# Kernel optimization log

Measured on AMD Instinct MI355X. Metric: run time of the kernel, lower is better.

Reference implementation:

```python
import jax, jax.numpy as jnp
import numpy as np

ALPHA = 0.15  # top-k fraction (forward default)


def setup_inputs() -> dict:
    key = jax.random.key(0)
    k1, k2, k3 = jax.random.split(key, 3)
    B, N, D = 8, 1024, 256
    x = jax.random.normal(k1, (B, N, D), dtype=jnp.float32)
    # torch nn.Linear(dim, H*head_dim, bias=False); stored here as [D, H*head_dim]
    W_src = jax.random.normal(k2, (D, D), dtype=jnp.float32) * (1.0 / np.sqrt(D))
    W_tgt = jax.random.normal(k3, (D, D), dtype=jnp.float32) * (1.0 / np.sqrt(D))
    return {"x": x, "W_src": W_src, "W_tgt": W_tgt}


def _topk_mask(adj, k):
    # adj: [B,H,N,N]; exact scatter of 1.0 at top-k indices along last axis
    B, H, N, _ = adj.shape
    _, idx = jax.lax.top_k(adj, k)              # [B,H,N,k]
    bi = jnp.arange(B)[:, None, None, None]
    hi = jnp.arange(H)[None, :, None, None]
    ni = jnp.arange(N)[None, None, :, None]
    mask = jnp.zeros_like(adj).at[bi, hi, ni, idx].set(1.0)
    return mask


def reference(x, W_src, W_tgt):
    # directed=True path of DirectedGraphLearner.forward
    B, N, D = x.shape
    H, head_dim = 4, D // 4
    k = max(1, int(ALPHA * N))
    src = (x @ W_src).reshape(B, N, H, head_dim)
    tgt = (x @ W_tgt).reshape(B, N, H, head_dim)
    adj = jnp.einsum('bihd,bjhd->bhij', src, tgt)
    adj = jax.nn.gelu(adj, approximate=False)    # torch F.gelu default = exact erf
    mask = _topk_mask(adj, k)
    return adj * mask
```

## Files before the change

kernel.cpp:

```cpp
#include <hip/hip_runtime.h>
#include <math.h>


#define KSEL 153u
#define EPSK 61000u

typedef __attribute__((ext_vector_type(8))) short short8v;
typedef __attribute__((ext_vector_type(4))) float float4v;

__device__ __forceinline__ float gelu_f32(float x) {
    return 0.5f * x * (1.0f + erff(x * 0.70710678118654752f));
}

__device__ __forceinline__ unsigned long long d2key(double v) {
    unsigned long long u = (unsigned long long)__double_as_longlong(v);
    return (u >> 63) ? ~u : (u | 0x8000000000000000ull);
}

__device__ __forceinline__ unsigned lkeyf(float v) {
    float q = fmaf(v, 33554432.0f, 2147483648.0f);
    q = fminf(fmaxf(q, 0.0f), 4294967040.0f);
    return (unsigned)q;
}

__device__ __forceinline__ unsigned short b16(float x) {
    unsigned u = __float_as_uint(x);
    u += 0x7FFFu + ((u >> 16) & 1u);
    return (unsigned short)(u >> 16);
}
__device__ __forceinline__ float bf2f(unsigned short h) {
    return __uint_as_float(((unsigned)h) << 16);
}
__device__ __forceinline__ unsigned pk2(float a, float b) {
    return (unsigned)b16(a) | ((unsigned)b16(b) << 16);
}

#define LGKM0()                                             \
    do {                                                    \
        asm volatile("s_waitcnt lgkmcnt(0)" ::: "memory");  \
        __builtin_amdgcn_sched_barrier(0);                  \
    } while (0)

template <bool W32>
__global__ __launch_bounds__(256) void k1_proj(const float* __restrict__ x,
                                               const float* __restrict__ Wsrc,
                                               const float* __restrict__ Wtgt,
                                               double* __restrict__ ws,
                                               unsigned short* __restrict__ th,
                                               unsigned short* __restrict__ tl) {
    __shared__ float xs[32 * 68];
    __shared__ float wsh[32 * 68];
    const int t = threadIdx.x;
    const int bx = blockIdx.x;
    const int by = blockIdx.y;
    const int col0 = (by & 3) * 64;
    const float* __restrict__ W = (by < 4) ? Wsrc : Wtgt;
    double* __restrict__ outp = ws + ((by < 4) ? 0 : 2097152);

    double acc[4][4];
#pragma unroll
    for (int i = 0; i < 4; ++i)
#pragma unroll
        for (int j = 0; j < 4; ++j) acc[i][j] = 0.0;

    const int m_loc = (t & 15) * 4;
    const int c_loc = (t >> 4) * 4;

    for (int kt = 0; kt < 8; ++kt) {
        __syncthreads();
#pragma unroll
        for (int it = 0; it < 2; ++it) {
            int f4 = t + 256 * it;
            int m = f4 >> 3, k4 = f4 & 7;
            float4 v = *reinterpret_cast<const float4*>(&x[(bx * 64 + m) * 256 + kt * 32 + 4 * k4]);
            xs[(4 * k4 + 0) * 68 + m] = v.x;
            xs[(4 * k4 + 1) * 68 + m] = v.y;
            xs[(4 * k4 + 2) * 68 + m] = v.z;
            xs[(4 * k4 + 3) * 68 + m] = v.w;
        }
#pragma unroll
        for (int it = 0; it < 2; ++it) {
            int f4 = t + 256 * it;
            int k = f4 >> 4, c4 = f4 & 15;
            *reinterpret_cast<float4*>(&wsh[k * 68 + 4 * c4]) =
                *reinterpret_cast<const float4*>(&W[(kt * 32 + k) * 256 + col0 + 4 * c4]);
        }
        __syncthreads();
#pragma unroll
        for (int kk = 0; kk < 32; ++kk) {
            float4 a = *reinterpret_cast<const float4*>(&xs[kk * 68 + m_loc]);
            float4 b = *reinterpret_cast<const float4*>(&wsh[kk * 68 + c_loc]);
            double ad[4] = {a.x, a.y, a.z, a.w};
            double bd[4] = {b.x, b.y, b.z, b.w};
#pragma unroll
            for (int i = 0; i < 4; ++i)
#pragma unroll
                for (int j = 0; j < 4; ++j) acc[i][j] += ad[i] * bd[j];
        }
    }
    const int hd = by & 3;
#pragma unroll
    for (int i = 0; i < 4; ++i) {
        int m = bx * 64 + m_loc + i;
        int b = m >> 10, n = m & 1023;
        int bhd = b * 4 + hd;
        size_t base = ((size_t)(bhd * 1024 + n)) * 64 + c_loc;
        double2 v01, v23;
        v01.x = acc[i][0]; v01.y = acc[i][1];
        v23.x = acc[i][2]; v23.y = acc[i][3];
        *reinterpret_cast<double2*>(&outp[base]) = v01;
        *reinterpret_cast<double2*>(&outp[base + 2]) = v23;
        if (W32 && by >= 4) {
            float f0 = (float)acc[i][0], f1 = (float)acc[i][1];
            float f2 = (float)acc[i][2], f3 = (float)acc[i][3];
            unsigned short h0 = b16(f0), h1 = b16(f1), h2 = b16(f2), h3 = b16(f3);
            uint2 H, L;
            H.x = (unsigned)h0 | ((unsigned)h1 << 16);
            H.y = (unsigned)h2 | ((unsigned)h3 << 16);
            L.x = pk2(f0 - bf2f(h0), f1 - bf2f(h1));
            L.y = pk2(f2 - bf2f(h2), f3 - bf2f(h3));
            int T = n >> 4, colLow = n & 15;
            int ks = c_loc >> 5, kg = (c_loc >> 3) & 3, elem = c_loc & 7;
            size_t fidx = ((size_t)bhd * 65536) +
                          (size_t)(((T * 2 + ks) * 64 + kg * 16 + colLow) * 8 + elem);
            *reinterpret_cast<uint2*>(&th[fidx]) = H;
            *reinterpret_cast<uint2*>(&tl[fidx]) = L;
        }
    }
}

template <bool FAST>
__global__ __launch_bounds__(256, 4) void k2a_gemm(const double* __restrict__ srcT,
                                                   const double* __restrict__ tgtT,
                                                   const unsigned short* __restrict__ th,
                                                   const unsigned short* __restrict__ tlo,
                                                   float* __restrict__ out) {
    __shared__ __align__(16) float tr[16 * 512];

    unsigned short* sHI = reinterpret_cast<unsigned short*>(tr);
    unsigned short* sLO = sHI + 1024;

    const int t = threadIdx.x;
    const int lane = t & 63;
    const int wv = t >> 6;
    const int bid = (blockIdx.x & 7) * 256 + (blockIdx.x >> 3);
    const int bh = bid >> 6;
    const int itile = bid & 63;
    const int row0 = itile * 16;
    const int r0 = 4 * wv;
    const size_t tgtBase = (size_t)bh * 65536;
    const unsigned short* __restrict__ thb = th + tgtBase;
    const unsigned short* __restrict__ tlb = tlo + tgtBase;

    {
        int r = t >> 4, dq = (t & 15) * 4;
        const double* sp = &srcT[((size_t)bh * 1024 + row0 + r) * 64 + dq];
        double2 a = *reinterpret_cast<const double2*>(sp);
        double2 b = *reinterpret_cast<const double2*>(sp + 2);
        float f0 = (float)a.x, f1 = (float)a.y, f2 = (float)b.x, f3 = (float)b.y;
        unsigned short h0 = b16(f0), h1 = b16(f1), h2 = b16(f2), h3 = b16(f3);
        int s = dq >> 3;
        int idx = r * 64 + ((s ^ (r & 7)) << 3) + (dq & 7);
        uint2 H, L;
        H.x = (unsigned)h0 | ((unsigned)h1 << 16);
        H.y = (unsigned)h2 | ((unsigned)h3 << 16);
        L.x = pk2(f0 - bf2f(h0), f1 - bf2f(h1));
        L.y = pk2(f2 - bf2f(h2), f3 - bf2f(h3));
        *reinterpret_cast<uint2*>(&sHI[idx]) = H;
        *reinterpret_cast<uint2*>(&sLO[idx]) = L;
    }
    __syncthreads();

    short8v Ah[2], Al[2];
#pragma unroll
    for (int ks = 0; ks < 2; ++ks) {
        int idxA = (lane & 15) * 64 + (((4 * ks + (lane >> 4)) ^ (lane & 7)) << 3);
        Ah[ks] = *reinterpret_cast<const short8v*>(&sHI[idxA]);
        Al[ks] = *reinterpret_cast<const short8v*>(&sLO[idxA]);
    }

    const int colA = lane & 15;
    const int kgrp = lane >> 4;
    const size_t outBase = ((size_t)bh * 1024 + row0 + r0) * 1024;

#pragma unroll
    for (int h = 0; h < 2; ++h) {
        float4v acc[8];
#pragma unroll
        for (int a = 0; a < 8; ++a) acc[a] = (float4v){0.f, 0.f, 0.f, 0.f};

#pragma unroll
        for (int u = 0; u < 8; ++u) {
            const int T = 32 * h + 4 * u + wv;
#pragma unroll
            for (int ks = 0; ks < 2; ++ks) {
                short8v Bh, Bl;
                if (FAST) {
                    const size_t fbase = (size_t)(((T * 2 + ks) * 64 + lane) * 8);
                    Bh = *reinterpret_cast<const short8v*>(&thb[fbase]);
                    Bl = *reinterpret_cast<const short8v*>(&tlb[fbase]);
                } else {
                    const size_t cbase = (size_t)(16 * T + colA) * 64 + kgrp * 8;
                    const double* gp = &tgtT[tgtBase + cbase + 32 * ks];
                    double2 d0 = *reinterpret_cast<const double2*>(gp);
                    double2 d1 = *reinterpret_cast<const double2*>(gp + 2);
                    double2 d2 = *reinterpret_cast<const double2*>(gp + 4);
                    double2 d3 = *reinterpret_cast<const double2*>(gp + 6);
                    float f[8] = {(float)d0.x, (float)d0.y, (float)d1.x, (float)d1.y,
                                  (float)d2.x, (float)d2.y, (float)d3.x, (float)d3.y};
                    unsigned short hh[8];
#pragma unroll
                    for (int e = 0; e < 8; ++e) hh[e] = b16(f[e]);
                    unsigned Hw[4], Lw[4];
#pragma unroll
                    for (int e = 0; e < 4; ++e) {
                        Hw[e] = (unsigned)hh[2 * e] | ((unsigned)hh[2 * e + 1] << 16);
                        Lw[e] = pk2(f[2 * e] - bf2f(hh[2 * e]), f[2 * e + 1] - bf2f(hh[2 * e + 1]));
                    }
                    Bh = *reinterpret_cast<const short8v*>(Hw);
                    Bl = *reinterpret_cast<const short8v*>(Lw);
                }
                acc[u] = __builtin_amdgcn_mfma_f32_16x16x32_bf16(Ah[ks], Bh, acc[u], 0, 0, 0);
                acc[u] = __builtin_amdgcn_mfma_f32_16x16x32_bf16(Al[ks], Bh, acc[u], 0, 0, 0);
                acc[u] = __builtin_amdgcn_mfma_f32_16x16x32_bf16(Ah[ks], Bl, acc[u], 0, 0, 0);
            }
        }

        __syncthreads();
#pragma unroll
        for (int u = 0; u < 8; ++u) {
            int colh = 16 * (4 * u + wv) + colA;
#pragma unroll
            for (int reg = 0; reg < 4; ++reg) {
                int row = 4 * kgrp + reg;
                tr[row * 512 + (colh ^ ((kgrp & 1) << 4))] = acc[u][reg];
            }
        }
        __syncthreads();
        const int rsw = (wv & 1) << 4;
#pragma unroll
        for (int ri = 0; ri < 4; ++ri) {
            int row = r0 + ri;
#pragma unroll
            for (int mm = 0; mm < 8; ++mm) {
                int colh = lane + 64 * mm;
                out[outBase + (size_t)ri * 1024 + 512 * h + colh] =
                    tr[row * 512 + (colh ^ rsw)];
            }
        }
    }
}

__global__ __launch_bounds__(256, 4) void k2b_select(const double* __restrict__ srcT,
                                                     const double* __restrict__ tgtT,
                                                     float* __restrict__ out) {
    __shared__ __align__(16) unsigned hist[4][256];

    const int t = threadIdx.x;
    const int lane = t & 63;
    const int wv = t >> 6;
    const int R = blockIdx.x * 4 + wv;
    const int bh = R >> 10;
    const size_t tgtBase = (size_t)bh * 65536;
    const size_t base = (size_t)R * 1024;

    float vals[16];
#pragma unroll
    for (int m = 0; m < 16; ++m) vals[m] = out[base + lane + 64 * m];

    unsigned* histw = hist[wv];
    unsigned* cjp = histw + 128;
    unsigned long long* ckp = reinterpret_cast<unsigned long long*>(histw);
    unsigned* ccp = histw + 192;

    unsigned ul[16];
#pragma unroll
    for (int m = 0; m < 16; ++m) ul[m] = lkeyf(vals[m]);

    unsigned prefA = 0u, maskA = 0u, rk = KSEL;
#pragma unroll 1
    for (int p = 1; p >= 0; --p) {
        const int sh = 16 + 8 * p;
        *reinterpret_cast<uint4*>(&histw[4 * lane]) = make_uint4(0u, 0u, 0u, 0u);
        LGKM0();
#pragma unroll
        for (int m = 0; m < 16; ++m) {
            if ((ul[m] & maskA) == prefA)
                atomicAdd(&histw[(ul[m] >> sh) & 255u], 1u);
        }
        LGKM0();
        unsigned h0 = histw[4 * lane + 0], h1 = histw[4 * lane + 1];
        unsigned h2 = histw[4 * lane + 2], h3 = histw[4 * lane + 3];
        unsigned S = h0 + h1 + h2 + h3;
        unsigned inc = S;
#pragma unroll
        for (int off = 1; off < 64; off <<= 1) {
            unsigned o = __shfl_down(inc, off, 64);
            inc = (lane + off < 64) ? (inc + o) : inc;
        }
        unsigned above = inc - S;
        bool found = (above < rk) && (rk <= inc);
        unsigned long long bal = __ballot(found);
        int L = __ffsll(bal) - 1;
        unsigned hh[4];
        hh[0] = __shfl(h0, L, 64);
        hh[1] = __shfl(h1, L, 64);
        hh[2] = __shfl(h2, L, 64);
        hh[3] = __shfl(h3, L, 64);
        unsigned cum = __shfl(above, L, 64);
        int bsel = -1;
#pragma unroll
        for (int q = 3; q >= 0; --q) {
            if (bsel < 0) {
                if (rk <= cum + hh[q]) {
                    bsel = q;
                    rk = rk - cum;
                } else {
                    cum += hh[q];
                }
            }
        }
        prefA |= (unsigned)(4 * L + bsel) << sh;
        maskA |= 0xFFu << sh;
    }

    const unsigned klo = prefA - EPSK;
    const unsigned khi = prefA + 65535u + EPSK;

    int ch = 0, cb = 0;
#pragma unroll
    for (int m = 0; m < 16; ++m) {
        ch += (ul[m] > khi) ? 1 : 0;
        cb += (ul[m] >= klo && ul[m] <= khi) ? 1 : 0;
    }
#pragma unroll
    for (int off = 32; off; off >>= 1) {
        ch += __shfl_xor(ch, off, 64);
        cb += __shfl_xor(cb, off, 64);
    }
    const unsigned need = KSEL - (unsigned)ch;
    const bool fastp = ((unsigned)cb == need);

    unsigned long long selMask = 0ull;
    unsigned cidx[16];
    if (!fastp) {
        if (lane == 0) *ccp = 0u;
        LGKM0();
#pragma unroll
        for (int m = 0; m < 16; ++m) {
            cidx[m] = 0xFFFFFFFFu;
            if (ul[m] >= klo && ul[m] <= khi) {
                unsigned idx = atomicAdd(ccp, 1u);
                cidx[m] = idx;
                if (idx < 64u) cjp[idx] = (unsigned)(lane + 64 * m);
            }
        }
        LGKM0();
        unsigned g = *ccp;
        if (g > 64u) g = 64u;
        unsigned rnk = need;
        if (lane < (int)g) {
            unsigned j = cjp[lane];
            const double2* sp = reinterpret_cast<const double2*>(&srcT[(size_t)R * 64]);
            const double2* tp = reinterpret_cast<const double2*>(&tgtT[tgtBase + (size_t)j * 64]);
            double a2 = 0.0;
#pragma unroll 8
            for (int d2 = 0; d2 < 32; ++d2) {
                double2 aa = sp[d2], bb = tp[d2];
                a2 = fma(aa.x, bb.x, fma(aa.y, bb.y, a2));
            }
            ckp[lane] = d2key(a2);
        }
        LGKM0();
        unsigned rnk2 = need;
        if (lane < (int)g) {
            unsigned long long myk = ckp[lane];
            unsigned myj = cjp[lane];
            rnk2 = 0;
            for (unsigned i = 0; i < g; ++i) {
                unsigned long long ki = ckp[i];
                rnk2 += (ki > myk || (ki == myk && cjp[i] < myj)) ? 1u : 0u;
            }
        }
        selMask = __ballot(lane < (int)g && rnk2 < need);
    }

#pragma unroll
    for (int m = 0; m < 16; ++m) {
        bool sel;
        if (ul[m] > khi) sel = true;
        else if (ul[m] < klo) sel = false;
        else sel = fastp ? true
                         : ((cidx[m] < 64u) ? (((selMask >> cidx[m]) & 1ull) != 0ull) : false);
        float v = vals[m];
        float g = 0.0f;
        if (sel) g = (v > 3.0f) ? v : gelu_f32(v);
        out[base + (unsigned)(lane + 64 * m)] = g;
    }
}

extern "C" void kernel_launch(void* const* d_in, const int* in_sizes, int n_in,
                              void* d_out, int out_size, void* d_ws, size_t ws_size,
                              hipStream_t stream) {
    const float* x = (const float*)d_in[0];
    const float* Wsrc = (const float*)d_in[1];
    const float* Wtgt = (const float*)d_in[2];
    float* out = (float*)d_out;
    double* ws = (double*)d_ws;
    unsigned short* th = (unsigned short*)((char*)d_ws + 33554432);
    unsigned short* tl = (unsigned short*)((char*)d_ws + 37748736);

    const bool fast = (ws_size >= 40u * 1024u * 1024u);
    dim3 g1(128, 8);
    if (fast) {
        k1_proj<true><<<g1, 256, 0, stream>>>(x, Wsrc, Wtgt, ws, th, tl);
        k2a_gemm<true><<<2048, 256, 0, stream>>>(ws, ws + 2097152, th, tl, out);
    } else {
        k1_proj<false><<<g1, 256, 0, stream>>>(x, Wsrc, Wtgt, ws, th, tl);
        k2a_gemm<false><<<2048, 256, 0, stream>>>(ws, ws + 2097152, th, tl, out);
    }
    k2b_select<<<8192, 256, 0, stream>>>(ws, ws + 2097152, out);
}
```

Measured before the change: 159.2 us.

## Store intermediate adjacency as int16 fixed-point and vectorize select IO

The GEMM kernel now writes its intermediate scores as 16-bit fixed-point (scale 512) into a workspace buffer instead of full fp32 into the output. The select kernel reads that compact buffer, widens the candidate window to absorb quantization error, and writes results with float4 stores in a contiguous-per-lane layout. The aim is to roughly halve the intermediate write and read traffic between the two kernels. It relies on exact fp64 re-ranking of boundary candidates for correctness. It requires a larger workspace and falls back to the fp32 path otherwise. The output values come from quantized scores, so precision is reduced to about 1/1024 and values beyond ±64 are clamped.

```diff
diff --git a/kernel.cpp b/kernel.cpp
--- a/kernel.cpp
+++ b/kernel.cpp
@@ -4,6 +4,7 @@
 
 #define KSEL 153u
 #define EPSK 61000u
+#define EPSKS 76000u
 
 typedef __attribute__((ext_vector_type(8))) short short8v;
 typedef __attribute__((ext_vector_type(4))) float float4v;
@@ -129,11 +130,12 @@
     }
 }
 
-template <bool FAST>
+template <bool FAST, bool S16>
 __global__ __launch_bounds__(256, 4) void k2a_gemm(const double* __restrict__ srcT,
                                                    const double* __restrict__ tgtT,
                                                    const unsigned short* __restrict__ th,
                                                    const unsigned short* __restrict__ tlo,
+                                                   short* __restrict__ adjS,
                                                    float* __restrict__ out) {
     __shared__ __align__(16) float tr[16 * 512];
 
@@ -181,7 +183,7 @@
 
     const int colA = lane & 15;
     const int kgrp = lane >> 4;
-    const size_t outBase = ((size_t)bh * 1024 + row0 + r0) * 1024;
+    const size_t rowG0 = (size_t)bh * 1024 + row0 + r0;
 
 #pragma unroll
     for (int h = 0; h < 2; ++h) {
@@ -242,17 +244,28 @@
         for (int ri = 0; ri < 4; ++ri) {
             int row = r0 + ri;
 #pragma unroll
-            for (int mm = 0; mm < 8; ++mm) {
-                int colh = lane + 64 * mm;
-                out[outBase + (size_t)ri * 1024 + 512 * h + colh] =
-                    tr[row * 512 + (colh ^ rsw)];
-            }
-        }
-    }
-}
-
+            for (int q = 0; q < 2; ++q) {
+                int colh = 4 * lane + 256 * q;
+                float4 v = *reinterpret_cast<const float4*>(&tr[row * 512 + (colh ^ rsw)]);
+                if (S16) {
+                    short4 s;
+                    s.x = (short)__float2int_rn(fminf(fmaxf(v.x * 512.f, -32767.f), 32767.f));
+                    s.y = (short)__float2int_rn(fminf(fmaxf(v.y * 512.f, -32767.f), 32767.f));
+                    s.z = (short)__float2int_rn(fminf(fmaxf(v.z * 512.f, -32767.f), 32767.f));
+                    s.w = (short)__float2int_rn(fminf(fmaxf(v.w * 512.f, -32767.f), 32767.f));
+                    *reinterpret_cast<short4*>(&adjS[(rowG0 + ri) * 1024 + 512 * h + colh]) = s;
+                } else {
+                    *reinterpret_cast<float4*>(&out[(rowG0 + ri) * 1024 + 512 * h + colh]) = v;
+                }
+            }
+        }
+    }
+}
+
+template <bool S16>
 __global__ __launch_bounds__(256, 4) void k2b_select(const double* __restrict__ srcT,
                                                      const double* __restrict__ tgtT,
+                                                     const short* __restrict__ adjS,
                                                      float* __restrict__ out) {
     __shared__ __align__(16) unsigned hist[4][256];
 
@@ -263,10 +276,26 @@
     const int bh = R >> 10;
     const size_t tgtBase = (size_t)bh * 65536;
     const size_t base = (size_t)R * 1024;
+    const unsigned eps = S16 ? EPSKS : EPSK;
 
     float vals[16];
-#pragma unroll
-    for (int m = 0; m < 16; ++m) vals[m] = out[base + lane + 64 * m];
+    if (S16) {
+#pragma unroll
+        for (int q = 0; q < 2; ++q) {
+            short8v s = *reinterpret_cast<const short8v*>(&adjS[base + 16 * lane + 8 * q]);
+#pragma unroll
+            for (int e = 0; e < 8; ++e) vals[8 * q + e] = (float)s[e] * (1.0f / 512.0f);
+        }
+    } else {
+#pragma unroll
+        for (int q = 0; q < 4; ++q) {
+            float4 v = *reinterpret_cast<const float4*>(&out[base + 16 * lane + 4 * q]);
+            vals[4 * q + 0] = v.x;
+            vals[4 * q + 1] = v.y;
+            vals[4 * q + 2] = v.z;
+            vals[4 * q + 3] = v.w;
+        }
+    }
 
     unsigned* histw = hist[wv];
     unsigned* cjp = histw + 128;
@@ -324,8 +353,8 @@
         maskA |= 0xFFu << sh;
     }
 
-    const unsigned klo = prefA - EPSK;
-    const unsigned khi = prefA + 65535u + EPSK;
+    const unsigned klo = prefA - eps;
+    const unsigned khi = prefA + 65535u + eps;
 
     int ch = 0, cb = 0;
 #pragma unroll
@@ -352,7 +381,7 @@
             if (ul[m] >= klo && ul[m] <= khi) {
                 unsigned idx = atomicAdd(ccp, 1u);
                 cidx[m] = idx;
-                if (idx < 64u) cjp[idx] = (unsigned)(lane + 64 * m);
+                if (idx < 64u) cjp[idx] = (unsigned)(16 * lane + m);
             }
         }
         LGKM0();
@@ -386,16 +415,21 @@
     }
 
 #pragma unroll
-    for (int m = 0; m < 16; ++m) {
-        bool sel;
-        if (ul[m] > khi) sel = true;
-        else if (ul[m] < klo) sel = false;
-        else sel = fastp ? true
-                         : ((cidx[m] < 64u) ? (((selMask >> cidx[m]) & 1ull) != 0ull) : false);
-        float v = vals[m];
-        float g = 0.0f;
-        if (sel) g = (v > 3.0f) ? v : gelu_f32(v);
-        out[base + (unsigned)(lane + 64 * m)] = g;
+    for (int q = 0; q < 4; ++q) {
+        float4 o;
+        float* op = &o.x;
+#pragma unroll
+        for (int e = 0; e < 4; ++e) {
+            int m = 4 * q + e;
+            bool sel;
+            if (ul[m] > khi) sel = true;
+            else if (ul[m] < klo) sel = false;
+            else sel = fastp ? true
+                             : ((cidx[m] < 64u) ? (((selMask >> cidx[m]) & 1ull) != 0ull) : false);
+            float v = vals[m];
+            op[e] = sel ? ((v > 3.0f) ? v : gelu_f32(v)) : 0.0f;
+        }
+        *reinterpret_cast<float4*>(&out[base + 16 * lane + 4 * q]) = o;
     }
 }
 
@@ -409,15 +443,22 @@
     double* ws = (double*)d_ws;
     unsigned short* th = (unsigned short*)((char*)d_ws + 33554432);
     unsigned short* tl = (unsigned short*)((char*)d_ws + 37748736);
+    short* adjS = (short*)((char*)d_ws + 41943040);
 
     const bool fast = (ws_size >= 40u * 1024u * 1024u);
+    const bool s16 = (ws_size >= 104u * 1024u * 1024u);
     dim3 g1(128, 8);
-    if (fast) {
+    if (fast && s16) {
         k1_proj<true><<<g1, 256, 0, stream>>>(x, Wsrc, Wtgt, ws, th, tl);
-        k2a_gemm<true><<<2048, 256, 0, stream>>>(ws, ws + 2097152, th, tl, out);
+        k2a_gemm<true, true><<<2048, 256, 0, stream>>>(ws, ws + 2097152, th, tl, adjS, out);
+        k2b_select<true><<<8192, 256, 0, stream>>>(ws, ws + 2097152, adjS, out);
+    } else if (fast) {
+        k1_proj<true><<<g1, 256, 0, stream>>>(x, Wsrc, Wtgt, ws, th, tl);
+        k2a_gemm<true, false><<<2048, 256, 0, stream>>>(ws, ws + 2097152, th, tl, adjS, out);
+        k2b_select<false><<<8192, 256, 0, stream>>>(ws, ws + 2097152, adjS, out);
     } else {
         k1_proj<false><<<g1, 256, 0, stream>>>(x, Wsrc, Wtgt, ws, th, tl);
-        k2a_gemm<false><<<2048, 256, 0, stream>>>(ws, ws + 2097152, th, tl, out);
-    }
-    k2b_select<<<8192, 256, 0, stream>>>(ws, ws + 2097152, out);
-}
+        k2a_gemm<false, false><<<2048, 256, 0, stream>>>(ws, ws + 2097152, th, tl, adjS, out);
+        k2b_select<false><<<8192, 256, 0, stream>>>(ws, ws + 2097152, adjS, out);
+    }
+}
```

After: 155.6 us. 2.3% less time.
